# Performance work log

Measured on AMD Instinct MI355X. Metric: run time of the kernel, lower is better.

## Reference

```python
import jax, jax.numpy as jnp
import numpy as np
from jax import lax

B, BANDS, HW = 128, 30, 15
DIM, NH, NC = 512, 8, 16
EPS = 1e-5

def _ln(x, w, b):
    m = x.mean(-1, keepdims=True)
    v = ((x - m) ** 2).mean(-1, keepdims=True)
    return (x - m) / jnp.sqrt(v + EPS) * w + b

def _bn(x, g, b, m, v):
    # eval-mode BatchNorm2d over NCHW
    inv = g / jnp.sqrt(v + EPS)
    return x * inv[None, :, None, None] + (b - m * inv)[None, :, None, None]

def _conv(x, w, b):
    y = lax.conv_general_dilated(x, w, (1, 1), 'SAME', dimension_numbers=('NCHW', 'OIHW', 'NCHW'))
    return y + b[None, :, None, None]

def _attn(x, qkv_w, qkv_b, proj_w, proj_b):
    Bq, N, C = x.shape
    hd = C // NH
    qkv = (x @ qkv_w.T + qkv_b).reshape(Bq, N, 3, NH, hd).transpose(2, 0, 3, 1, 4)
    q, k, v = qkv[0], qkv[1], qkv[2]
    a = jax.nn.softmax(jnp.einsum('bhnd,bhmd->bhnm', q, k) * (hd ** -0.5), axis=-1)
    o = jnp.einsum('bhnm,bhmd->bhnd', a, v).transpose(0, 2, 1, 3).reshape(Bq, N, C)
    return o @ proj_w.T + proj_b

def _mlp(x, w1, b1, w2, b2):
    return jax.nn.gelu(x @ w1.T + b1, approximate=False) @ w2.T + b2

def _forward(x, conv_h_w, conv_h_b, bn_h_g, bn_h_b, bn_h_m, bn_h_v, cnn_conv_w, cnn_conv_b, cnn_bn_g, cnn_bn_b, cnn_bn_m, cnn_bn_v, cnn_fc_w, cnn_fc_b, spa_cls, spe_cls, spa_pos, spe_pos, blk_n1_w, blk_n1_b, blk_n2_w, blk_n2_b, blk_qkv_w, blk_qkv_b, blk_proj_w, blk_proj_b, blk_fc1_w, blk_fc1_b, blk_fc2_w, blk_fc2_b, norm1_w, norm1_b, norm2_w, norm2_b, head_w, head_b):
    x = x[:, 0]  # squeeze(1) -> [B, BANDS, H, W]
    Bn = x.shape[0]
    # --- spatial stream ---
    h = jax.nn.relu(_bn(_conv(x, conv_h_w, conv_h_b), bn_h_g, bn_h_b, bn_h_m, bn_h_v))
    spa = h.reshape(Bn, DIM, -1).transpose(0, 2, 1)  # b (h w) c
    spa = jnp.concatenate([jnp.broadcast_to(spa_cls, (Bn, 1, DIM)), spa], axis=1) + spa_pos
    # --- spectral stream: per-band CNN batched across bands in one pass ---
    bands = x.reshape(Bn * BANDS, 1, HW, HW)
    f = jax.nn.relu(_bn(_conv(bands, cnn_conv_w, cnn_conv_b), cnn_bn_g, cnn_bn_b, cnn_bn_m, cnn_bn_v))
    f = f.mean(axis=(2, 3))  # adaptive avg pool to 1x1
    f = jax.nn.relu(f @ cnn_fc_w.T + cnn_fc_b).reshape(Bn, BANDS, DIM)
    spe = jnp.concatenate([jnp.broadcast_to(spe_cls, (Bn, 1, DIM)), f], axis=1) + spe_pos
    xs, ys = spa, spe
    for i in range(2):  # CTMF blocks (eval: drop_path/dropout are identity)
        xin = _ln(jnp.concatenate([ys[:, :1], xs[:, 1:]], axis=1), blk_n1_w[i], blk_n1_b[i])
        yin = _ln(jnp.concatenate([xs[:, :1], ys[:, 1:]], axis=1), blk_n1_w[i], blk_n1_b[i])
        x_ = _attn(xin, blk_qkv_w[i], blk_qkv_b[i], blk_proj_w[i], blk_proj_b[i])
        y_ = _attn(yin, blk_qkv_w[i], blk_qkv_b[i], blk_proj_w[i], blk_proj_b[i])
        xs2 = xs + jnp.concatenate([xs[:, :1] + y_[:, :1], x_[:, 1:]], axis=1)
        ys2 = ys + jnp.concatenate([ys[:, :1] + x_[:, :1], y_[:, 1:]], axis=1)
        xs = xs2 + _mlp(_ln(xs2, blk_n2_w[i], blk_n2_b[i]), blk_fc1_w[i], blk_fc1_b[i], blk_fc2_w[i], blk_fc2_b[i])
        ys = ys2 + _mlp(_ln(ys2, blk_n2_w[i], blk_n2_b[i]), blk_fc1_w[i], blk_fc1_b[i], blk_fc2_w[i], blk_fc2_b[i])
    cls = jnp.concatenate([_ln(xs[:, 0], norm1_w, norm1_b), _ln(ys[:, 0], norm2_w, norm2_b)], axis=-1)
    return cls @ head_w.T + head_b

def setup_inputs() -> dict:
    key = jax.random.key(0)
    ks = jax.random.split(key, 32)
    r = lambda i, shape, s=0.02: jax.random.normal(ks[i], shape, dtype=jnp.float32) * s
    Nspa = HW * HW + 1
    Nspe = BANDS + 1
    return {
        'x': jax.random.normal(ks[0], (B, 1, BANDS, HW, HW), dtype=jnp.float32),
        'conv_h_w': r(1, (DIM, BANDS, 3, 3)),
        'conv_h_b': jnp.zeros((DIM,), jnp.float32),
        'bn_h_g': 1.0 + r(2, (DIM,)),
        'bn_h_b': r(3, (DIM,)),
        'bn_h_m': r(4, (DIM,), 0.1),
        'bn_h_v': 0.5 + jax.random.uniform(ks[5], (DIM,), dtype=jnp.float32),
        'cnn_conv_w': r(6, (128, 1, 3, 3), 0.1),
        'cnn_conv_b': jnp.zeros((128,), jnp.float32),
        'cnn_bn_g': 1.0 + r(7, (128,)),
        'cnn_bn_b': r(8, (128,)),
        'cnn_bn_m': r(9, (128,), 0.1),
        'cnn_bn_v': 0.5 + jax.random.uniform(ks[10], (128,), dtype=jnp.float32),
        'cnn_fc_w': r(11, (DIM, 128)),
        'cnn_fc_b': jnp.zeros((DIM,), jnp.float32),
        'spa_cls': jnp.zeros((1, 1, DIM), jnp.float32),
        'spe_cls': jnp.zeros((1, 1, DIM), jnp.float32),
        'spa_pos': r(12, (1, Nspa, DIM)),
        'spe_pos': r(13, (1, Nspe, DIM)),
        'blk_n1_w': jnp.ones((2, DIM), jnp.float32),
        'blk_n1_b': jnp.zeros((2, DIM), jnp.float32),
        'blk_n2_w': jnp.ones((2, DIM), jnp.float32),
        'blk_n2_b': jnp.zeros((2, DIM), jnp.float32),
        'blk_qkv_w': r(14, (2, 3 * DIM, DIM)),
        'blk_qkv_b': jnp.zeros((2, 3 * DIM), jnp.float32),
        'blk_proj_w': r(15, (2, DIM, DIM)),
        'blk_proj_b': jnp.zeros((2, DIM), jnp.float32),
        'blk_fc1_w': r(16, (2, DIM, DIM)),
        'blk_fc1_b': jnp.zeros((2, DIM), jnp.float32),
        'blk_fc2_w': r(17, (2, DIM, DIM)),
        'blk_fc2_b': jnp.zeros((2, DIM), jnp.float32),
        'norm1_w': jnp.ones((DIM,), jnp.float32),
        'norm1_b': jnp.zeros((DIM,), jnp.float32),
        'norm2_w': jnp.ones((DIM,), jnp.float32),
        'norm2_b': jnp.zeros((DIM,), jnp.float32),
        'head_w': r(18, (NC, 2 * DIM)),
        'head_b': jnp.zeros((NC,), jnp.float32),
    }

def reference(x, conv_h_w, conv_h_b, bn_h_g, bn_h_b, bn_h_m, bn_h_v, cnn_conv_w, cnn_conv_b, cnn_bn_g, cnn_bn_b, cnn_bn_m, cnn_bn_v, cnn_fc_w, cnn_fc_b, spa_cls, spe_cls, spa_pos, spe_pos, blk_n1_w, blk_n1_b, blk_n2_w, blk_n2_b, blk_qkv_w, blk_qkv_b, blk_proj_w, blk_proj_b, blk_fc1_w, blk_fc1_b, blk_fc2_w, blk_fc2_b, norm1_w, norm1_b, norm2_w, norm2_b, head_w, head_b):
    return _forward(x, conv_h_w, conv_h_b, bn_h_g, bn_h_b, bn_h_m, bn_h_v, cnn_conv_w, cnn_conv_b, cnn_bn_g, cnn_bn_b, cnn_bn_m, cnn_bn_v, cnn_fc_w, cnn_fc_b, spa_cls, spe_cls, spa_pos, spe_pos, blk_n1_w, blk_n1_b, blk_n2_w, blk_n2_b, blk_qkv_w, blk_qkv_b, blk_proj_w, blk_proj_b, blk_fc1_w, blk_fc1_b, blk_fc2_w, blk_fc2_b, norm1_w, norm1_b, norm2_w, norm2_b, head_w, head_b)
```

## Files before the change

### kernel.cpp

```cpp
#include <hip/hip_runtime.h>
#include <hip/hip_bf16.h>

typedef unsigned short u16;
typedef __attribute__((ext_vector_type(8))) short bf16x8;
typedef __attribute__((ext_vector_type(4))) float f32x4;

#define NB 128
#define BANDS 30
#define HWD 15
#define NPIX 225
#define DIMC 512
#define NHEAD 8
#define HD 64
#define NSPA 226
#define NSPE 31
#define EPSF 1e-5f
#define KCONV 320
#define MXROWS 28928
#define MYROWS 3968
#define M2ROWS 32896

__device__ __forceinline__ float b2f(u16 u) { return __uint_as_float(((unsigned)u) << 16); }
__device__ __forceinline__ u16 f2b(float f) {
  __hip_bfloat16 h = __float2bfloat16(f);
  return *reinterpret_cast<u16*>(&h);
}

#if __has_builtin(__builtin_amdgcn_global_load_lds)
#define HAVE_GLDS 1
__device__ __forceinline__ void gl_lds16(const void* g, void* l) {
  __builtin_amdgcn_global_load_lds((const __attribute__((address_space(1))) void*)g,
                                   (__attribute__((address_space(3))) void*)l, 16, 0, 0);
}
#else
#define HAVE_GLDS 0
#endif

__global__ __launch_bounds__(256) void cvt_k(const float* __restrict__ s, u16* __restrict__ d, int n) {
  for (int i = blockIdx.x * 256 + threadIdx.x; i < n; i += gridDim.x * 256) d[i] = f2b(s[i]);
}

__global__ __launch_bounds__(256) void convw_k(const float* __restrict__ w, u16* __restrict__ d) {
  int i = blockIdx.x * 256 + threadIdx.x;
  if (i >= DIMC * KCONV) return;
  int r = i / KCONV, c = i - r * KCONV;
  d[i] = (c < 270) ? f2b(w[r * 270 + c]) : (u16)0;
}

__global__ __launch_bounds__(256) void bnprep_k(const float* __restrict__ g, const float* __restrict__ bb,
    const float* __restrict__ bm, const float* __restrict__ bv, const float* __restrict__ cb,
    float* __restrict__ sc, float* __restrict__ sh) {
  int n = blockIdx.x * 256 + threadIdx.x;
  if (n < DIMC) {
    float inv = g[n] * rsqrtf(bv[n] + EPSF);
    sc[n] = inv;
    sh[n] = (cb[n] - bm[n]) * inv + bb[n];
  }
}

__global__ __launch_bounds__(256) void im2col_k(const float* __restrict__ x, u16* __restrict__ Ac) {
  int idx = blockIdx.x * 256 + threadIdx.x;
  if (idx >= 28800 * 40) return;
  int m = idx / 40, g = idx - m * 40;
  int b = m / NPIX, p = m - b * NPIX;
  int i = p / 15, j = p - i * 15;
  union { u16 v[8]; uint4 u; } out;
#pragma unroll
  for (int e = 0; e < 8; e++) {
    int c = g * 8 + e;
    float v = 0.f;
    if (c < 270) {
      int band = c / 9, q = c - band * 9;
      int di = q / 3, dj = q - di * 3;
      int ii = i + di - 1, jj = j + dj - 1;
      if ((unsigned)ii < 15u && (unsigned)jj < 15u)
        v = x[((size_t)b * BANDS + band) * NPIX + ii * 15 + jj];
    }
    out.v[e] = f2b(v);
  }
  *reinterpret_cast<uint4*>(Ac + (size_t)m * KCONV + g * 8) = out.u;
}

__global__ __launch_bounds__(256) void cls_init_k(const float* __restrict__ spa_cls,
    const float* __restrict__ spe_cls, const float* __restrict__ spa_pos,
    const float* __restrict__ spe_pos, float* __restrict__ xs, float* __restrict__ ys) {
  int b = blockIdx.x, t = threadIdx.x;
  int d0 = t, d1 = t + 256;
  xs[(size_t)b * NSPA * DIMC + d0] = spa_cls[d0] + spa_pos[d0];
  xs[(size_t)b * NSPA * DIMC + d1] = spa_cls[d1] + spa_pos[d1];
  ys[(size_t)b * NSPE * DIMC + d0] = spe_cls[d0] + spe_pos[d0];
  ys[(size_t)b * NSPE * DIMC + d1] = spe_cls[d1] + spe_pos[d1];
}

__global__ __launch_bounds__(256) void cnn_conv_k(const float* __restrict__ x,
    const float* __restrict__ w, const float* __restrict__ cb, const float* __restrict__ g,
    const float* __restrict__ bb, const float* __restrict__ bm, const float* __restrict__ bv,
    u16* __restrict__ pooled) {
  __shared__ float img[2][NPIX];
  int b0 = blockIdx.x * 2;
  int t = threadIdx.x;
  for (int idx = t; idx < 2 * NPIX; idx += 256) ((float*)img)[idx] = x[(size_t)b0 * NPIX + idx];
  __syncthreads();
  int half = t >> 7, ch = t & 127;
  const float* im = img[half];
  float inv = g[ch] * rsqrtf(bv[ch] + EPSF);
  float beta = bb[ch] - bm[ch] * inv;
  float w9[9];
#pragma unroll
  for (int q = 0; q < 9; q++) w9[q] = w[ch * 9 + q] * inv;
  float bias = cb[ch] * inv + beta;

  float rm[15], rc[15], rp[15];
#pragma unroll
  for (int j = 0; j < 15; j++) { rm[j] = 0.f; rc[j] = im[j]; }
  float sum = 0.f;
  for (int i = 0; i < 15; i++) {
#pragma unroll
    for (int j = 0; j < 15; j++) rp[j] = (i < 14) ? im[(i + 1) * 15 + j] : 0.f;
    float a[15];
#pragma unroll
    for (int j = 0; j < 15; j++) a[j] = fmaf(w9[4], rc[j], bias);
#pragma unroll
    for (int j = 0; j < 15; j++) {
      if (j > 0)  a[j] = fmaf(w9[3], rc[j - 1], a[j]);
      if (j < 14) a[j] = fmaf(w9[5], rc[j + 1], a[j]);
      a[j] = fmaf(w9[1], rm[j], a[j]);
      if (j > 0)  a[j] = fmaf(w9[0], rm[j - 1], a[j]);
      if (j < 14) a[j] = fmaf(w9[2], rm[j + 1], a[j]);
      a[j] = fmaf(w9[7], rp[j], a[j]);
      if (j > 0)  a[j] = fmaf(w9[6], rp[j - 1], a[j]);
      if (j < 14) a[j] = fmaf(w9[8], rp[j + 1], a[j]);
    }
#pragma unroll
    for (int j = 0; j < 15; j++) sum += fmaxf(a[j], 0.f);
#pragma unroll
    for (int j = 0; j < 15; j++) { rm[j] = rc[j]; rc[j] = rp[j]; }
  }
  pooled[(size_t)(b0 + half) * 128 + ch] = f2b(sum * (1.0f / 225.0f));
}

template <int GATHER>
__global__ __launch_bounds__(256) void ln_v_k(const float* __restrict__ xsc,
    const float* __restrict__ w, const float* __restrict__ bprm, u16* __restrict__ out) {
  int wid = threadIdx.x >> 6, lane = threadIdx.x & 63;
  int row = blockIdx.x * 4 + wid;
  const float* src;
  if (GATHER) {
    if (row < MXROWS) {
      int b = row / NSPA, tk = row - b * NSPA;
      src = (tk == 0) ? xsc + ((size_t)MXROWS + (size_t)b * NSPE) * DIMC
                      : xsc + (size_t)row * DIMC;
    } else {
      int ry = row - MXROWS;
      int b = ry / NSPE, tk = ry - b * NSPE;
      src = (tk == 0) ? xsc + (size_t)b * NSPA * DIMC : xsc + (size_t)row * DIMC;
    }
  } else {
    src = xsc + (size_t)row * DIMC;
  }
  float4 a0 = *reinterpret_cast<const float4*>(src + lane * 8);
  float4 a1 = *reinterpret_cast<const float4*>(src + lane * 8 + 4);
  float s = a0.x + a0.y + a0.z + a0.w + a1.x + a1.y + a1.z + a1.w;
  float sq = a0.x * a0.x + a0.y * a0.y + a0.z * a0.z + a0.w * a0.w +
             a1.x * a1.x + a1.y * a1.y + a1.z * a1.z + a1.w * a1.w;
#pragma unroll
  for (int off = 1; off <= 32; off <<= 1) { s += __shfl_xor(s, off); sq += __shfl_xor(sq, off); }
  float mean = s * (1.0f / 512.0f);
  float var = sq * (1.0f / 512.0f) - mean * mean;
  float rstd = rsqrtf(var + EPSF);
  float4 w0 = *reinterpret_cast<const float4*>(w + lane * 8);
  float4 w1 = *reinterpret_cast<const float4*>(w + lane * 8 + 4);
  float4 b0 = *reinterpret_cast<const float4*>(bprm + lane * 8);
  float4 b1 = *reinterpret_cast<const float4*>(bprm + lane * 8 + 4);
  union { u16 v[8]; uint4 u; } r;
  r.v[0] = f2b((a0.x - mean) * rstd * w0.x + b0.x);
  r.v[1] = f2b((a0.y - mean) * rstd * w0.y + b0.y);
  r.v[2] = f2b((a0.z - mean) * rstd * w0.z + b0.z);
  r.v[3] = f2b((a0.w - mean) * rstd * w0.w + b0.w);
  r.v[4] = f2b((a1.x - mean) * rstd * w1.x + b1.x);
  r.v[5] = f2b((a1.y - mean) * rstd * w1.y + b1.y);
  r.v[6] = f2b((a1.z - mean) * rstd * w1.z + b1.z);
  r.v[7] = f2b((a1.w - mean) * rstd * w1.w + b1.w);
  *reinterpret_cast<uint4*>(out + (size_t)row * DIMC + lane * 8) = r.u;
}

__global__ __launch_bounds__(256) void ln_cls_k(const float* __restrict__ xs,
    const float* __restrict__ ys, const float* __restrict__ w1, const float* __restrict__ b1,
    const float* __restrict__ w2, const float* __restrict__ b2, float* __restrict__ cls) {
  int gb = blockIdx.x;
  int half = gb & 1, b = gb >> 1;
  const float* src = half ? (ys + (size_t)b * NSPE * DIMC) : (xs + (size_t)b * NSPA * DIMC);
  const float* w = half ? w2 : w1;
  const float* bp = half ? b2 : b1;
  int t = threadIdx.x;
  float x0 = src[t], x1 = src[t + 256];
  float s = x0 + x1, sq = x0 * x0 + x1 * x1;
  for (int off = 32; off; off >>= 1) { s += __shfl_down(s, off); sq += __shfl_down(sq, off); }
  __shared__ float sa[4], sb4[4];
  int wid = t >> 6;
  if ((t & 63) == 0) { sa[wid] = s; sb4[wid] = sq; }
  __syncthreads();
  s = sa[0] + sa[1] + sa[2] + sa[3];
  sq = sb4[0] + sb4[1] + sb4[2] + sb4[3];
  float mean = s * (1.0f / 512.0f);
  float var = sq * (1.0f / 512.0f) - mean * mean;
  float rstd = rsqrtf(var + EPSF);
  cls[(size_t)b * 1024 + half * DIMC + t] = (x0 - mean) * rstd * w[t] + bp[t];
  cls[(size_t)b * 1024 + half * DIMC + t + 256] = (x1 - mean) * rstd * w[t + 256] + bp[t + 256];
}

template <int MODE>
__global__ __launch_bounds__(256) void mgemm_k(const u16* __restrict__ A, const u16* __restrict__ Bw,
    const float* __restrict__ bias, float* outf, u16* outb, int M, int N, int K,
    const float* aux0, const float* aux1, const float* aux2) {
  __shared__ u16 As[128 * 64];
  __shared__ u16 Bs[128 * 64];
  const int t = threadIdx.x;
  const int wid = t >> 6, l = t & 63;
  const int wm = wid >> 1, wn = wid & 1;
  const int fr = l & 15, kg = l >> 4;

  const int nx = gridDim.x, nwg = nx * gridDim.y;
  int hlin = blockIdx.y * nx + blockIdx.x;
  int xcd = hlin & 7, j = hlin >> 3;
  int q8 = nwg >> 3, r8 = nwg & 7;
  int L = (xcd < r8 ? xcd * (q8 + 1) : r8 * (q8 + 1) + (xcd - r8) * q8) + j;
  const int n0 = (L % nx) * 128, m0 = (L / nx) * 128;

  const int srow = l >> 3;
  const int sslot = l & 7;

  f32x4 acc[4][4];
#pragma unroll
  for (int i = 0; i < 4; i++)
#pragma unroll
    for (int j2 = 0; j2 < 4; j2++) acc[i][j2] = (f32x4){0.f, 0.f, 0.f, 0.f};

  for (int kq = 0; kq < K; kq += 64) {
#if !HAVE_GLDS
    uint4 ra[4], rb[4];
#pragma unroll
    for (int i = 0; i < 4; i++) {
      int r = wid * 32 + i * 8 + srow;
      int cg = sslot ^ (r & 7);
      ra[i] = *reinterpret_cast<const uint4*>(A + (size_t)(m0 + r) * K + kq + cg * 8);
      rb[i] = *reinterpret_cast<const uint4*>(Bw + (size_t)(n0 + r) * K + kq + cg * 8);
    }
#endif
    __syncthreads();
#if HAVE_GLDS
#pragma unroll
    for (int i = 0; i < 4; i++) {
      int r = wid * 32 + i * 8 + srow;
      int cg = sslot ^ (r & 7);
      gl_lds16(A + (size_t)(m0 + r) * K + kq + cg * 8, &As[(wid * 32 + i * 8) * 64]);
      gl_lds16(Bw + (size_t)(n0 + r) * K + kq + cg * 8, &Bs[(wid * 32 + i * 8) * 64]);
    }
#else
#pragma unroll
    for (int i = 0; i < 4; i++) {
      int r = wid * 32 + i * 8 + srow;
      *reinterpret_cast<uint4*>(&As[r * 64 + sslot * 8]) = ra[i];
      *reinterpret_cast<uint4*>(&Bs[r * 64 + sslot * 8]) = rb[i];
    }
#endif
    __syncthreads();
#pragma unroll
    for (int h = 0; h < 2; h++) {
      bf16x8 af[4], bfr[4];
#pragma unroll
      for (int mi = 0; mi < 4; mi++) {
        int r = wm * 64 + mi * 16 + fr;
        af[mi] = *reinterpret_cast<const bf16x8*>(&As[r * 64 + (((h * 4 + kg) ^ (fr & 7)) * 8)]);
      }
#pragma unroll
      for (int nj = 0; nj < 4; nj++) {
        int n = wn * 64 + nj * 16 + fr;
        bfr[nj] = *reinterpret_cast<const bf16x8*>(&Bs[n * 64 + (((h * 4 + kg) ^ (fr & 7)) * 8)]);
      }
#pragma unroll
      for (int mi = 0; mi < 4; mi++)
#pragma unroll
        for (int nj = 0; nj < 4; nj++)
          acc[mi][nj] = __builtin_amdgcn_mfma_f32_16x16x32_bf16(af[mi], bfr[nj], acc[mi][nj], 0, 0, 0);
    }
  }

#pragma unroll
  for (int mi = 0; mi < 4; mi++) {
#pragma unroll
    for (int q = 0; q < 4; q++) {
      int m = m0 + wm * 64 + mi * 16 + kg * 4 + q;
#pragma unroll
      for (int nj = 0; nj < 4; nj++) {
        int n = n0 + wn * 64 + nj * 16 + fr;
        float v = acc[mi][nj][q];
        if (MODE == 0) {
          outb[(size_t)m * N + n] = f2b(v + bias[n]);
        } else if (MODE == 1) {
          float z = v + bias[n];
          outb[(size_t)m * N + n] = f2b(0.5f * z * (1.0f + erff(z * 0.70710678118f)));
        } else if (MODE == 2) {
          size_t idx = (size_t)m * N + n;
          outf[idx] = v + bias[n] + aux0[idx];
        } else if (MODE == 3) {
          int b = m / NPIX, p = m - b * NPIX;
          float z = fmaxf(v * aux0[n] + aux1[n], 0.f) + aux2[(size_t)(p + 1) * DIMC + n];
          outf[((size_t)b * NSPA + p + 1) * DIMC + n] = z;
        } else if (MODE == 4) {
          int b = m / BANDS, band = m - b * BANDS;
          float z = fmaxf(v + bias[n], 0.f) + aux0[(size_t)(band + 1) * DIMC + n];
          outf[((size_t)b * NSPE + band + 1) * DIMC + n] = z;
        } else if (MODE == 5) {
          float z = v + bias[n];
          int tk, sidx;
          if (m < MXROWS) {
            int b = m / NSPA; tk = m - b * NSPA; sidx = b;
          } else {
            int ry = m - MXROWS; int b = ry / NSPE; tk = ry - b * NSPE; sidx = 128 + b;
          }
          if (tk == 0) outb[(size_t)sidx * DIMC + n] = f2b(z);
          else outf[(size_t)m * N + n] += z;
        }
      }
    }
  }
}

__global__ __launch_bounds__(256) void cls_swap_k(float* __restrict__ xsc,
                                                  const u16* __restrict__ clsprj) {
  int b = blockIdx.x, t = threadIdx.x;
  size_t xrow = (size_t)b * NSPA * DIMC;
  size_t yrow = ((size_t)MXROWS + (size_t)b * NSPE) * DIMC;
#pragma unroll
  for (int q = 0; q < 2; q++) {
    int d = t + q * 256;
    xsc[xrow + d] = 2.0f * xsc[xrow + d] + b2f(clsprj[(size_t)(128 + b) * DIMC + d]);
    xsc[yrow + d] = 2.0f * xsc[yrow + d] + b2f(clsprj[(size_t)b * DIMC + d]);
  }
}

template <int NTOK, int KP>
__global__ __launch_bounds__(256) void vt_k(const u16* __restrict__ qkv, u16* __restrict__ vtout) {
  __shared__ u16 Vl[64 * 72];
  int h = blockIdx.x, b = blockIdx.y;
  int t = threadIdx.x;
  const size_t rs = 3 * DIMC;
  const u16* src = qkv + (size_t)b * NTOK * rs + 2 * DIMC + h * HD;
  u16* dst = vtout + (size_t)(b * NHEAD + h) * HD * KP;
  for (int kt = 0; kt < KP / 64; kt++) {
    __syncthreads();
#pragma unroll
    for (int p = 0; p < 2; p++) {
      int idx = p * 256 + t;
      int row = idx >> 3, c = idx & 7;
      int tok = kt * 64 + row;
      uint4 v = make_uint4(0, 0, 0, 0);
      if (tok < NTOK) v = *reinterpret_cast<const uint4*>(src + (size_t)tok * rs + c * 8);
      *reinterpret_cast<uint4*>(&Vl[row * 72 + c * 8]) = v;
    }
    __syncthreads();
    int d = t & 63, tg = t >> 6;
    unsigned pu[8];
#pragma unroll
    for (int i = 0; i < 8; i++) {
      unsigned a = Vl[(tg * 16 + 2 * i) * 72 + d];
      unsigned bb2 = Vl[(tg * 16 + 2 * i + 1) * 72 + d];
      pu[i] = (bb2 << 16) | a;
    }
    uint4 o0 = make_uint4(pu[0], pu[1], pu[2], pu[3]);
    uint4 o1 = make_uint4(pu[4], pu[5], pu[6], pu[7]);
    u16* dp = dst + (size_t)d * KP + kt * 64 + tg * 16;
    *reinterpret_cast<uint4*>(dp) = o0;
    *reinterpret_cast<uint4*>(dp + 8) = o1;
  }
}

__device__ __forceinline__ int fsw(int row, int chunk) {
  return row * 64 + ((chunk ^ (row & 7)) << 3);
}
__device__ __forceinline__ void stage64(const u16* __restrict__ gsrc, size_t gstride,
                                        u16* lds, int w, int l) {
#pragma unroll
  for (int i = 0; i < 2; i++) {
    int r = w * 16 + i * 8 + (l >> 3);
    int c = l & 7;
    int scg = c ^ (r & 7);
    const u16* g = gsrc + (size_t)r * gstride + scg * 8;
#if HAVE_GLDS
    gl_lds16(g, &lds[(w * 16 + i * 8) * 64]);
#else
    *reinterpret_cast<uint4*>(&lds[r * 64 + c * 8]) = *reinterpret_cast<const uint4*>(g);
#endif
  }
}

__global__ __launch_bounds__(256) void flashq_k(const u16* __restrict__ qkv,
    const u16* __restrict__ vt, u16* __restrict__ o, int N, int kpad, float scale) {
  __shared__ u16 Qs[4][64 * 64];
  __shared__ u16 KV[2][64 * 64];
  u16* Ks = KV[0];
  u16* Vs = KV[1];
  u16* Ol = KV[0];
  const int h = blockIdx.x, b = blockIdx.y;
  const int t = threadIdx.x;
  const int w = t >> 6, l = t & 63;
  const int lr = l & 15, lk = l >> 4;
  const size_t rs = 3 * DIMC;
  const size_t qbase = (size_t)b * N * rs + h * HD;
  const u16* vbase = vt + (size_t)(b * NHEAD + h) * HD * kpad;

#pragma unroll
  for (int i = 0; i < 8; i++) {
    int r = i * 8 + (l >> 3);
    int c = l & 7;
    int scg = c ^ (r & 7);
    const u16* g = qkv + qbase + (size_t)(w * 64 + r) * rs + scg * 8;
#if HAVE_GLDS
    gl_lds16(g, &Qs[w][(i * 8) * 64]);
#else
    *reinterpret_cast<uint4*>(&Qs[w][r * 64 + c * 8]) = *reinterpret_cast<const uint4*>(g);
#endif
  }
  __syncthreads();
  bf16x8 bq[4][2];
#pragma unroll
  for (int nj = 0; nj < 4; nj++) {
    bq[nj][0] = *reinterpret_cast<const bf16x8*>(&Qs[w][fsw(nj * 16 + lr, lk)]);
    bq[nj][1] = *reinterpret_cast<const bf16x8*>(&Qs[w][fsw(nj * 16 + lr, 4 + lk)]);
  }

  float m_i[4], l_i[4];
  f32x4 oacc[4][4];
#pragma unroll
  for (int nj = 0; nj < 4; nj++) { m_i[nj] = -1e30f; l_i[nj] = 0.f; }
#pragma unroll
  for (int mi = 0; mi < 4; mi++)
#pragma unroll
    for (int nj = 0; nj < 4; nj++) oacc[mi][nj] = (f32x4){0.f, 0.f, 0.f, 0.f};

  const int nkt = kpad >> 6;
  for (int kt = 0; kt < nkt; kt++) {
    __syncthreads();
    stage64(qkv + qbase + DIMC + (size_t)(kt * 64) * rs, rs, Ks, w, l);
    stage64(vbase + kt * 64, (size_t)kpad, Vs, w, l);
    __syncthreads();

#pragma unroll
    for (int nj = 0; nj < 4; nj++) {
      f32x4 st[4];
#pragma unroll
      for (int mi = 0; mi < 4; mi++) st[mi] = (f32x4){0.f, 0.f, 0.f, 0.f};
      __builtin_amdgcn_s_setprio(1);
#pragma unroll
      for (int mi = 0; mi < 4; mi++) {
        bf16x8 ak0 = *reinterpret_cast<const bf16x8*>(&Ks[fsw(mi * 16 + lr, lk)]);
        bf16x8 ak1 = *reinterpret_cast<const bf16x8*>(&Ks[fsw(mi * 16 + lr, 4 + lk)]);
        st[mi] = __builtin_amdgcn_mfma_f32_16x16x32_bf16(ak0, bq[nj][0], st[mi], 0, 0, 0);
        st[mi] = __builtin_amdgcn_mfma_f32_16x16x32_bf16(ak1, bq[nj][1], st[mi], 0, 0, 0);
      }
      __builtin_amdgcn_s_setprio(0);

      float sv[4][4];
      float tmax = -1e30f;
#pragma unroll
      for (int mi = 0; mi < 4; mi++)
#pragma unroll
        for (int q = 0; q < 4; q++) {
          int kgl = kt * 64 + mi * 16 + lk * 4 + q;
          float v = (kgl < N) ? st[mi][q] * scale : -1e30f;
          sv[mi][q] = v;
          tmax = fmaxf(tmax, v);
        }
      tmax = fmaxf(tmax, __shfl_xor(tmax, 16));
      tmax = fmaxf(tmax, __shfl_xor(tmax, 32));
      float mn = fmaxf(m_i[nj], tmax);
      float corr = __expf(m_i[nj] - mn);
      m_i[nj] = mn;
      float rsum = 0.f;
#pragma unroll
      for (int mi = 0; mi < 4; mi++)
#pragma unroll
        for (int q = 0; q < 4; q++) {
          float p = __expf(sv[mi][q] - mn);
          sv[mi][q] = p;
          rsum += p;
        }
      rsum += __shfl_xor(rsum, 16);
      rsum += __shfl_xor(rsum, 32);
      l_i[nj] = l_i[nj] * corr + rsum;
#pragma unroll
      for (int mi = 0; mi < 4; mi++) oacc[mi][nj] *= corr;

      unsigned pk[4][2];
#pragma unroll
      for (int mi = 0; mi < 4; mi++) {
        pk[mi][0] = ((unsigned)f2b(sv[mi][1]) << 16) | (unsigned)f2b(sv[mi][0]);
        pk[mi][1] = ((unsigned)f2b(sv[mi][3]) << 16) | (unsigned)f2b(sv[mi][2]);
      }
      int src0 = lr + 32 * (lk & 1);
      int src1 = src0 + 16;
      bool hi = lk >= 2;
      bf16x8 pbv[2];
#pragma unroll
      for (int c = 0; c < 2; c++) {
        unsigned a0 = __shfl(pk[2 * c][0], src0), b0 = __shfl(pk[2 * c + 1][0], src0);
        unsigned a1 = __shfl(pk[2 * c][1], src0), b1 = __shfl(pk[2 * c + 1][1], src0);
        unsigned a2 = __shfl(pk[2 * c][0], src1), b2 = __shfl(pk[2 * c + 1][0], src1);
        unsigned a3 = __shfl(pk[2 * c][1], src1), b3 = __shfl(pk[2 * c + 1][1], src1);
        union { unsigned u[4]; bf16x8 v; } pu;
        pu.u[0] = hi ? b0 : a0;
        pu.u[1] = hi ? b1 : a1;
        pu.u[2] = hi ? b2 : a2;
        pu.u[3] = hi ? b3 : a3;
        pbv[c] = pu.v;
      }

      __builtin_amdgcn_s_setprio(1);
#pragma unroll
      for (int mi = 0; mi < 4; mi++) {
        bf16x8 av0 = *reinterpret_cast<const bf16x8*>(&Vs[fsw(mi * 16 + lr, lk)]);
        bf16x8 av1 = *reinterpret_cast<const bf16x8*>(&Vs[fsw(mi * 16 + lr, 4 + lk)]);
        oacc[mi][nj] = __builtin_amdgcn_mfma_f32_16x16x32_bf16(av0, pbv[0], oacc[mi][nj], 0, 0, 0);
        oacc[mi][nj] = __builtin_amdgcn_mfma_f32_16x16x32_bf16(av1, pbv[1], oacc[mi][nj], 0, 0, 0);
      }
      __builtin_amdgcn_s_setprio(0);
    }
  }

  float invl[4];
#pragma unroll
  for (int nj = 0; nj < 4; nj++) invl[nj] = 1.0f / l_i[nj];
  for (int pass = 0; pass < 4; pass++) {
    __syncthreads();
    if (w == pass) {
#pragma unroll
      for (int mi = 0; mi < 4; mi++)
#pragma unroll
        for (int nj = 0; nj < 4; nj++) {
          unsigned lo = ((unsigned)f2b(oacc[mi][nj][1] * invl[nj]) << 16) |
                        (unsigned)f2b(oacc[mi][nj][0] * invl[nj]);
          unsigned hi2 = ((unsigned)f2b(oacc[mi][nj][3] * invl[nj]) << 16) |
                         (unsigned)f2b(oacc[mi][nj][2] * invl[nj]);
          uint2 pr; pr.x = lo; pr.y = hi2;
          *reinterpret_cast<uint2*>(&Ol[(nj * 16 + lr) * 72 + mi * 16 + lk * 4]) = pr;
        }
    }
    __syncthreads();
    int row = t >> 2, c4 = t & 3;
    int qrow = pass * 64 + row;
    if (qrow < N) {
      uint4 v0 = *reinterpret_cast<const uint4*>(&Ol[row * 72 + c4 * 8]);
      uint4 v1 = *reinterpret_cast<const uint4*>(&Ol[row * 72 + (c4 + 4) * 8]);
      u16* op = o + ((size_t)b * N + qrow) * DIMC + h * HD;
      *reinterpret_cast<uint4*>(op + c4 * 8) = v0;
      *reinterpret_cast<uint4*>(op + (c4 + 4) * 8) = v1;
    }
  }
}

__global__ __launch_bounds__(256) void flashm_k(const u16* __restrict__ qkv,
    const u16* __restrict__ vt, u16* __restrict__ o, int N, int kpad, float scale) {
  __shared__ u16 Qs[64 * 64], Ks[64 * 64], Vs[64 * 64];
  __shared__ u16 Ol[64 * 72];
  const int qt = blockIdx.x, h = blockIdx.y, b = blockIdx.z;
  const int t = threadIdx.x;
  const int w = t >> 6, l = t & 63;
  const int lr = l & 15, lk = l >> 4;
  const size_t rs = 3 * DIMC;
  const size_t qbase = (size_t)b * N * rs + h * HD;
  const u16* vbase = vt + (size_t)(b * NHEAD + h) * HD * kpad;

  stage64(qkv + qbase + (size_t)(qt * 64) * rs, rs, Qs, w, l);
  __syncthreads();
  bf16x8 bq0 = *reinterpret_cast<const bf16x8*>(&Qs[fsw(w * 16 + lr, lk)]);
  bf16x8 bq1 = *reinterpret_cast<const bf16x8*>(&Qs[fsw(w * 16 + lr, 4 + lk)]);

  float m_i = -1e30f, l_i = 0.f;
  f32x4 oacc[4];
#pragma unroll
  for (int mi = 0; mi < 4; mi++) oacc[mi] = (f32x4){0.f, 0.f, 0.f, 0.f};

  const int nkt = (kpad + 63) >> 6;
  for (int kt = 0; kt < nkt; kt++) {
    __syncthreads();
    stage64(qkv + qbase + DIMC + (size_t)(kt * 64) * rs, rs, Ks, w, l);
    stage64(vbase + kt * 64, (size_t)kpad, Vs, w, l);
    __syncthreads();

    f32x4 st[4];
#pragma unroll
    for (int mi = 0; mi < 4; mi++) st[mi] = (f32x4){0.f, 0.f, 0.f, 0.f};
#pragma unroll
    for (int mi = 0; mi < 4; mi++) {
      bf16x8 ak0 = *reinterpret_cast<const bf16x8*>(&Ks[fsw(mi * 16 + lr, lk)]);
      bf16x8 ak1 = *reinterpret_cast<const bf16x8*>(&Ks[fsw(mi * 16 + lr, 4 + lk)]);
      st[mi] = __builtin_amdgcn_mfma_f32_16x16x32_bf16(ak0, bq0, st[mi], 0, 0, 0);
      st[mi] = __builtin_amdgcn_mfma_f32_16x16x32_bf16(ak1, bq1, st[mi], 0, 0, 0);
    }

    float sv[4][4];
    float tmax = -1e30f;
#pragma unroll
    for (int mi = 0; mi < 4; mi++)
#pragma unroll
      for (int q = 0; q < 4; q++) {
        int kgl = kt * 64 + mi * 16 + lk * 4 + q;
        float v = (kgl < N) ? st[mi][q] * scale : -1e30f;
        sv[mi][q] = v;
        tmax = fmaxf(tmax, v);
      }
    tmax = fmaxf(tmax, __shfl_xor(tmax, 16));
    tmax = fmaxf(tmax, __shfl_xor(tmax, 32));
    float mn = fmaxf(m_i, tmax);
    float corr = __expf(m_i - mn);
    m_i = mn;
    float rsum = 0.f;
#pragma unroll
    for (int mi = 0; mi < 4; mi++)
#pragma unroll
      for (int q = 0; q < 4; q++) {
        float p = __expf(sv[mi][q] - mn);
        sv[mi][q] = p;
        rsum += p;
      }
    rsum += __shfl_xor(rsum, 16);
    rsum += __shfl_xor(rsum, 32);
    l_i = l_i * corr + rsum;
#pragma unroll
    for (int mi = 0; mi < 4; mi++) oacc[mi] *= corr;

    unsigned pk[4][2];
#pragma unroll
    for (int mi = 0; mi < 4; mi++) {
      pk[mi][0] = ((unsigned)f2b(sv[mi][1]) << 16) | (unsigned)f2b(sv[mi][0]);
      pk[mi][1] = ((unsigned)f2b(sv[mi][3]) << 16) | (unsigned)f2b(sv[mi][2]);
    }
    int src0 = lr + 32 * (lk & 1);
    int src1 = src0 + 16;
    bool hi = lk >= 2;
    bf16x8 pbv[2];
#pragma unroll
    for (int c = 0; c < 2; c++) {
      unsigned a0 = __shfl(pk[2 * c][0], src0), b0 = __shfl(pk[2 * c + 1][0], src0);
      unsigned a1 = __shfl(pk[2 * c][1], src0), b1 = __shfl(pk[2 * c + 1][1], src0);
      unsigned a2 = __shfl(pk[2 * c][0], src1), b2 = __shfl(pk[2 * c + 1][0], src1);
      unsigned a3 = __shfl(pk[2 * c][1], src1), b3 = __shfl(pk[2 * c + 1][1], src1);
      union { unsigned u[4]; bf16x8 v; } pu;
      pu.u[0] = hi ? b0 : a0;
      pu.u[1] = hi ? b1 : a1;
      pu.u[2] = hi ? b2 : a2;
      pu.u[3] = hi ? b3 : a3;
      pbv[c] = pu.v;
    }

#pragma unroll
    for (int mi = 0; mi < 4; mi++) {
      bf16x8 av0 = *reinterpret_cast<const bf16x8*>(&Vs[fsw(mi * 16 + lr, lk)]);
      bf16x8 av1 = *reinterpret_cast<const bf16x8*>(&Vs[fsw(mi * 16 + lr, 4 + lk)]);
      oacc[mi] = __builtin_amdgcn_mfma_f32_16x16x32_bf16(av0, pbv[0], oacc[mi], 0, 0, 0);
      oacc[mi] = __builtin_amdgcn_mfma_f32_16x16x32_bf16(av1, pbv[1], oacc[mi], 0, 0, 0);
    }
  }

  float invl = 1.0f / l_i;
#pragma unroll
  for (int mi = 0; mi < 4; mi++) {
    unsigned lo = ((unsigned)f2b(oacc[mi][1] * invl) << 16) | (unsigned)f2b(oacc[mi][0] * invl);
    unsigned hi2 = ((unsigned)f2b(oacc[mi][3] * invl) << 16) | (unsigned)f2b(oacc[mi][2] * invl);
    uint2 pr; pr.x = lo; pr.y = hi2;
    *reinterpret_cast<uint2*>(&Ol[(w * 16 + lr) * 72 + mi * 16 + lk * 4]) = pr;
  }
  __syncthreads();
  {
    int row = t >> 2, c4 = t & 3;
    int qrow = qt * 64 + row;
    if (qrow < N) {
      uint4 v0 = *reinterpret_cast<const uint4*>(&Ol[row * 72 + c4 * 8]);
      uint4 v1 = *reinterpret_cast<const uint4*>(&Ol[row * 72 + (c4 + 4) * 8]);
      u16* op = o + ((size_t)b * N + qrow) * DIMC + h * HD;
      *reinterpret_cast<uint4*>(op + c4 * 8) = v0;
      *reinterpret_cast<uint4*>(op + (c4 + 4) * 8) = v1;
    }
  }
}

__global__ __launch_bounds__(256) void head_k(const float* __restrict__ cls,
    const float* __restrict__ hw, const float* __restrict__ hb, float* __restrict__ out) {
  __shared__ float cl[1024];
  __shared__ float part[256];
  int b = blockIdx.x, t = threadIdx.x;
  for (int idx = t; idx < 1024; idx += 256) cl[idx] = cls[(size_t)b * 1024 + idx];
  __syncthreads();
  int c = t >> 4, sl = t & 15;
  float p = 0.f;
  for (int j = 0; j < 64; j++) p += cl[sl * 64 + j] * hw[(size_t)c * 1024 + sl * 64 + j];
  part[t] = p;
  __syncthreads();
  if (sl == 0) {
    float sum = hb[c];
    for (int q = 0; q < 16; q++) sum += part[c * 16 + q];
    out[(size_t)b * 16 + c] = sum;
  }
}

extern "C" void kernel_launch(void* const* d_in, const int* in_sizes, int n_in,
                              void* d_out, int out_size, void* d_ws, size_t ws_size,
                              hipStream_t stream) {
  const float* x        = (const float*)d_in[0];
  const float* conv_h_w = (const float*)d_in[1];
  const float* conv_h_b = (const float*)d_in[2];
  const float* bn_h_g   = (const float*)d_in[3];
  const float* bn_h_b   = (const float*)d_in[4];
  const float* bn_h_m   = (const float*)d_in[5];
  const float* bn_h_v   = (const float*)d_in[6];
  const float* cnn_conv_w = (const float*)d_in[7];
  const float* cnn_conv_b = (const float*)d_in[8];
  const float* cnn_bn_g = (const float*)d_in[9];
  const float* cnn_bn_b = (const float*)d_in[10];
  const float* cnn_bn_m = (const float*)d_in[11];
  const float* cnn_bn_v = (const float*)d_in[12];
  const float* cnn_fc_w = (const float*)d_in[13];
  const float* cnn_fc_b = (const float*)d_in[14];
  const float* spa_cls  = (const float*)d_in[15];
  const float* spe_cls  = (const float*)d_in[16];
  const float* spa_pos  = (const float*)d_in[17];
  const float* spe_pos  = (const float*)d_in[18];
  const float* blk_n1_w = (const float*)d_in[19];
  const float* blk_n1_b = (const float*)d_in[20];
  const float* blk_n2_w = (const float*)d_in[21];
  const float* blk_n2_b = (const float*)d_in[22];
  const float* blk_qkv_w = (const float*)d_in[23];
  const float* blk_qkv_b = (const float*)d_in[24];
  const float* blk_proj_w = (const float*)d_in[25];
  const float* blk_proj_b = (const float*)d_in[26];
  const float* blk_fc1_w = (const float*)d_in[27];
  const float* blk_fc1_b = (const float*)d_in[28];
  const float* blk_fc2_w = (const float*)d_in[29];
  const float* blk_fc2_b = (const float*)d_in[30];
  const float* norm1_w  = (const float*)d_in[31];
  const float* norm1_b  = (const float*)d_in[32];
  const float* norm2_w  = (const float*)d_in[33];
  const float* norm2_b  = (const float*)d_in[34];
  const float* head_w   = (const float*)d_in[35];
  const float* head_b   = (const float*)d_in[36];

  char* ws = (char*)d_ws;
  size_t off = 0;
  auto take = [&](size_t bytes) -> char* {
    char* p = ws + off;
    off = (off + bytes + 255) & ~(size_t)255;
    return p;
  };
  const int Mx = MXROWS, M2 = M2ROWS;
  const int Mc = NB * NPIX;
  const int Mf = NB * BANDS;
  float* xsc  = (float*)take((size_t)M2 * DIMC * 4);
  float* ysb  = xsc + (size_t)Mx * DIMC;
  u16* xyin   = (u16*)take((size_t)M2 * DIMC * 2);
  u16* qkvxy  = (u16*)take((size_t)M2 * 3 * DIMC * 2);
  u16* oxy    = (u16*)take((size_t)M2 * DIMC * 2);
  u16* clsprj = (u16*)take((size_t)256 * DIMC * 2);
  float* clsb = (float*)take((size_t)NB * 1024 * 4);
  u16* pooled = (u16*)take((size_t)Mf * 128 * 2);
  u16* qkvWb  = (u16*)take((size_t)2 * 3 * DIMC * DIMC * 2);
  u16* projWb = (u16*)take((size_t)2 * DIMC * DIMC * 2);
  u16* fc1Wb  = (u16*)take((size_t)2 * DIMC * DIMC * 2);
  u16* fc2Wb  = (u16*)take((size_t)2 * DIMC * DIMC * 2);
  u16* fcWb   = (u16*)take((size_t)DIMC * 128 * 2);
  u16* convWb = (u16*)take((size_t)DIMC * KCONV * 2);
  float* bnsc = (float*)take(DIMC * 4);
  float* bnsh = (float*)take(DIMC * 4);
  u16* vty    = (u16*)take((size_t)NB * NHEAD * HD * 64 * 2);
  u16* Acol   = qkvxy;
  u16* vtx    = xyin;

  cvt_k<<<1024, 256, 0, stream>>>(blk_qkv_w, qkvWb, 2 * 3 * DIMC * DIMC);
  cvt_k<<<1024, 256, 0, stream>>>(blk_proj_w, projWb, 2 * DIMC * DIMC);
  cvt_k<<<1024, 256, 0, stream>>>(blk_fc1_w, fc1Wb, 2 * DIMC * DIMC);
  cvt_k<<<1024, 256, 0, stream>>>(blk_fc2_w, fc2Wb, 2 * DIMC * DIMC);
  cvt_k<<<256, 256, 0, stream>>>(cnn_fc_w, fcWb, DIMC * 128);
  convw_k<<<(DIMC * KCONV + 255) / 256, 256, 0, stream>>>(conv_h_w, convWb);
  bnprep_k<<<2, 256, 0, stream>>>(bn_h_g, bn_h_b, bn_h_m, bn_h_v, conv_h_b, bnsc, bnsh);

  cls_init_k<<<NB, 256, 0, stream>>>(spa_cls, spe_cls, spa_pos, spe_pos, xsc, ysb);
  im2col_k<<<(Mc * 40 + 255) / 256, 256, 0, stream>>>(x, Acol);
  mgemm_k<3><<<dim3(4, Mc / 128), 256, 0, stream>>>(Acol, convWb, nullptr, xsc, nullptr,
      Mc, DIMC, KCONV, bnsc, bnsh, spa_pos);
  cnn_conv_k<<<Mf / 2, 256, 0, stream>>>(x, cnn_conv_w, cnn_conv_b, cnn_bn_g, cnn_bn_b,
                                         cnn_bn_m, cnn_bn_v, pooled);
  mgemm_k<4><<<dim3(4, Mf / 128), 256, 0, stream>>>(pooled, fcWb, cnn_fc_b, ysb, nullptr,
      Mf, DIMC, 128, spe_pos, nullptr, nullptr);

  for (int i = 0; i < 2; i++) {
    const float* n1w = blk_n1_w + i * DIMC;
    const float* n1b = blk_n1_b + i * DIMC;
    const float* n2w = blk_n2_w + i * DIMC;
    const float* n2b = blk_n2_b + i * DIMC;
    const u16* qkvW = qkvWb + (size_t)i * 3 * DIMC * DIMC;
    const float* qkvB = blk_qkv_b + (size_t)i * 3 * DIMC;
    const u16* projW = projWb + (size_t)i * DIMC * DIMC;
    const float* projB = blk_proj_b + (size_t)i * DIMC;
    const u16* fc1W = fc1Wb + (size_t)i * DIMC * DIMC;
    const float* fc1B = blk_fc1_b + (size_t)i * DIMC;
    const u16* fc2W = fc2Wb + (size_t)i * DIMC * DIMC;
    const float* fc2B = blk_fc2_b + (size_t)i * DIMC;

    ln_v_k<1><<<M2 / 4, 256, 0, stream>>>(xsc, n1w, n1b, xyin);

    mgemm_k<0><<<dim3(12, M2 / 128), 256, 0, stream>>>(xyin, qkvW, qkvB, nullptr, qkvxy,
        M2, 3 * DIMC, DIMC, nullptr, nullptr, nullptr);

    vt_k<NSPA, 256><<<dim3(NHEAD, NB), 256, 0, stream>>>(qkvxy, vtx);
    vt_k<NSPE, 64><<<dim3(NHEAD, NB), 256, 0, stream>>>(qkvxy + (size_t)Mx * 3 * DIMC, vty);

    flashq_k<<<dim3(NHEAD, NB), 256, 0, stream>>>(qkvxy, vtx, oxy, NSPA, 256, 0.125f);
    flashm_k<<<dim3(1, NHEAD, NB), 256, 0, stream>>>(qkvxy + (size_t)Mx * 3 * DIMC, vty,
                                                     oxy + (size_t)Mx * DIMC, NSPE, 64, 0.125f);

    mgemm_k<5><<<dim3(4, M2 / 128), 256, 0, stream>>>(oxy, projW, projB, xsc, clsprj,
        M2, DIMC, DIMC, nullptr, nullptr, nullptr);
    cls_swap_k<<<NB, 256, 0, stream>>>(xsc, clsprj);

    ln_v_k<0><<<M2 / 4, 256, 0, stream>>>(xsc, n2w, n2b, xyin);
    mgemm_k<1><<<dim3(4, M2 / 128), 256, 0, stream>>>(xyin, fc1W, fc1B, nullptr, qkvxy,
        M2, DIMC, DIMC, nullptr, nullptr, nullptr);
    mgemm_k<2><<<dim3(4, M2 / 128), 256, 0, stream>>>(qkvxy, fc2W, fc2B, xsc, nullptr,
        M2, DIMC, DIMC, xsc, nullptr, nullptr);
  }

  ln_cls_k<<<NB * 2, 256, 0, stream>>>(xsc, ysb, norm1_w, norm1_b, norm2_w, norm2_b, clsb);
  head_k<<<NB, 256, 0, stream>>>(clsb, head_w, head_b, (float*)d_out);
}
```

Measured before the change: 830.7 us.

## Add 256x256-tile double-buffered GEMM kernel for transformer block matmuls

Adds a new g256_k GEMM with 256x256 output tiles, 512 threads and an XCD-aware block remapping. It uses double-buffered LDS staging through global_load_lds with an XOR-swizzled layout and raised wave priority around the MFMA loop. The QKV, projection, fc1 and fc2 GEMMs now use it instead of the 128-tile mgemm_k, and their epilogue modes move into the new kernel. The aim is more data reuse per tile and less global traffic. In exchange, activation buffers are padded to a multiple of 256 rows, and the large LDS footprint limits each CU to one block, with a partial wave on the N=512 GEMMs.

New measurement: 1.204 ms. 44.9% more time.

```diff
diff --git a/kernel.cpp b/kernel.cpp
--- a/kernel.cpp
+++ b/kernel.cpp
@@ -19,6 +19,7 @@
 #define MXROWS 28928
 #define MYROWS 3968
 #define M2ROWS 32896
+#define M2PAD 33024
 
 __device__ __forceinline__ float b2f(u16 u) { return __uint_as_float(((unsigned)u) << 16); }
 __device__ __forceinline__ u16 f2b(float f) {
@@ -295,15 +296,7 @@
       for (int nj = 0; nj < 4; nj++) {
         int n = n0 + wn * 64 + nj * 16 + fr;
         float v = acc[mi][nj][q];
-        if (MODE == 0) {
-          outb[(size_t)m * N + n] = f2b(v + bias[n]);
-        } else if (MODE == 1) {
-          float z = v + bias[n];
-          outb[(size_t)m * N + n] = f2b(0.5f * z * (1.0f + erff(z * 0.70710678118f)));
-        } else if (MODE == 2) {
-          size_t idx = (size_t)m * N + n;
-          outf[idx] = v + bias[n] + aux0[idx];
-        } else if (MODE == 3) {
+        if (MODE == 3) {
           int b = m / NPIX, p = m - b * NPIX;
           float z = fmaxf(v * aux0[n] + aux1[n], 0.f) + aux2[(size_t)(p + 1) * DIMC + n];
           outf[((size_t)b * NSPA + p + 1) * DIMC + n] = z;
@@ -311,16 +304,132 @@
           int b = m / BANDS, band = m - b * BANDS;
           float z = fmaxf(v + bias[n], 0.f) + aux0[(size_t)(band + 1) * DIMC + n];
           outf[((size_t)b * NSPE + band + 1) * DIMC + n] = z;
-        } else if (MODE == 5) {
-          float z = v + bias[n];
-          int tk, sidx;
-          if (m < MXROWS) {
-            int b = m / NSPA; tk = m - b * NSPA; sidx = b;
-          } else {
-            int ry = m - MXROWS; int b = ry / NSPE; tk = ry - b * NSPE; sidx = 128 + b;
+        }
+      }
+    }
+  }
+}
+
+template <int MODE>
+__global__ __launch_bounds__(512, 2) void g256_k(const u16* __restrict__ A,
+    const u16* __restrict__ Bw, const float* __restrict__ bias, float* outf, u16* outb,
+    int M, int N, int K, const float* aux0) {
+  __shared__ u16 As[2][256 * 64];
+  __shared__ u16 Bs[2][256 * 64];
+  const int t = threadIdx.x;
+  const int w = t >> 6, l = t & 63;
+  const int wm = w >> 2, wn = w & 3;
+  const int fr = l & 15, kg = l >> 4;
+
+  const int nx = gridDim.x, nwg = nx * gridDim.y;
+  int hlin = blockIdx.y * nx + blockIdx.x;
+  int xcd = hlin & 7, jj = hlin >> 3;
+  int q8 = nwg >> 3, r8 = nwg & 7;
+  int L = (xcd < r8 ? xcd * (q8 + 1) : r8 * (q8 + 1) + (xcd - r8) * q8) + jj;
+  const int n0 = (L % nx) * 256, m0 = (L / nx) * 256;
+
+  const int srow = l >> 3;
+  const int sslot = l & 7;
+  const int scg = sslot ^ srow;
+
+  f32x4 acc[8][4];
+#pragma unroll
+  for (int i = 0; i < 8; i++)
+#pragma unroll
+    for (int j2 = 0; j2 < 4; j2++) acc[i][j2] = (f32x4){0.f, 0.f, 0.f, 0.f};
+
+  const int nkt = K >> 6;
+
+  auto STAGE = [&](int buf, int kt) {
+    const int kq = kt * 64;
+#pragma unroll
+    for (int i = 0; i < 4; i++) {
+      int rb = w * 32 + i * 8;
+#if HAVE_GLDS
+      gl_lds16(A + (size_t)(m0 + rb + srow) * K + kq + scg * 8, &As[buf][rb * 64]);
+      gl_lds16(Bw + (size_t)(n0 + rb + srow) * K + kq + scg * 8, &Bs[buf][rb * 64]);
+#else
+      *reinterpret_cast<uint4*>(&As[buf][(rb + srow) * 64 + scg * 8]) =
+          *reinterpret_cast<const uint4*>(A + (size_t)(m0 + rb + srow) * K + kq + sslot * 8);
+      *reinterpret_cast<uint4*>(&Bs[buf][(rb + srow) * 64 + scg * 8]) =
+          *reinterpret_cast<const uint4*>(Bw + (size_t)(n0 + rb + srow) * K + kq + sslot * 8);
+#endif
+    }
+  };
+
+  STAGE(0, 0);
+  STAGE(1, 1);
+  asm volatile("s_waitcnt vmcnt(8)" ::: "memory");
+  __builtin_amdgcn_s_barrier();
+
+  for (int kt = 0; kt < nkt; kt++) {
+    const int buf = kt & 1;
+    const u16* Ab = As[buf];
+    const u16* Bb = Bs[buf];
+#pragma unroll
+    for (int kh = 0; kh < 2; kh++) {
+      bf16x8 af[8], bfr[4];
+#pragma unroll
+      for (int mi = 0; mi < 8; mi++) {
+        int r = wm * 128 + mi * 16 + fr;
+        af[mi] = *reinterpret_cast<const bf16x8*>(&Ab[r * 64 + (((kh * 4 + kg) ^ (fr & 7)) << 3)]);
+      }
+#pragma unroll
+      for (int nj = 0; nj < 4; nj++) {
+        int n = wn * 64 + nj * 16 + fr;
+        bfr[nj] = *reinterpret_cast<const bf16x8*>(&Bb[n * 64 + (((kh * 4 + kg) ^ (fr & 7)) << 3)]);
+      }
+      __builtin_amdgcn_s_setprio(1);
+#pragma unroll
+      for (int mi = 0; mi < 8; mi++)
+#pragma unroll
+        for (int nj = 0; nj < 4; nj++)
+          acc[mi][nj] = __builtin_amdgcn_mfma_f32_16x16x32_bf16(af[mi], bfr[nj], acc[mi][nj], 0, 0, 0);
+      __builtin_amdgcn_s_setprio(0);
+    }
+    asm volatile("s_waitcnt lgkmcnt(0)" ::: "memory");
+    __builtin_amdgcn_sched_barrier(0);
+    __builtin_amdgcn_s_barrier();
+    if (kt + 2 < nkt) STAGE(buf, kt + 2);
+    if (kt + 1 < nkt) {
+      if (kt + 2 < nkt) {
+        asm volatile("s_waitcnt vmcnt(8)" ::: "memory");
+      } else {
+        asm volatile("s_waitcnt vmcnt(0)" ::: "memory");
+      }
+      __builtin_amdgcn_s_barrier();
+    }
+  }
+
+#pragma unroll
+  for (int mi = 0; mi < 8; mi++) {
+#pragma unroll
+    for (int q = 0; q < 4; q++) {
+      int m = m0 + wm * 128 + mi * 16 + kg * 4 + q;
+      if (m < M) {
+#pragma unroll
+        for (int nj = 0; nj < 4; nj++) {
+          int n = n0 + wn * 64 + nj * 16 + fr;
+          float v = acc[mi][nj][q];
+          if (MODE == 0) {
+            outb[(size_t)m * N + n] = f2b(v + bias[n]);
+          } else if (MODE == 1) {
+            float z = v + bias[n];
+            outb[(size_t)m * N + n] = f2b(0.5f * z * (1.0f + erff(z * 0.70710678118f)));
+          } else if (MODE == 2) {
+            size_t idx = (size_t)m * N + n;
+            outf[idx] = v + bias[n] + aux0[idx];
+          } else if (MODE == 5) {
+            float z = v + bias[n];
+            int tk, sidx;
+            if (m < MXROWS) {
+              int b = m / NSPA; tk = m - b * NSPA; sidx = b;
+            } else {
+              int ry = m - MXROWS; int b = ry / NSPE; tk = ry - b * NSPE; sidx = 128 + b;
+            }
+            if (tk == 0) outb[(size_t)sidx * DIMC + n] = f2b(z);
+            else outf[(size_t)m * N + n] += z;
           }
-          if (tk == 0) outb[(size_t)sidx * DIMC + n] = f2b(z);
-          else outf[(size_t)m * N + n] += z;
         }
       }
     }
@@ -757,9 +866,9 @@
   const int Mf = NB * BANDS;
   float* xsc  = (float*)take((size_t)M2 * DIMC * 4);
   float* ysb  = xsc + (size_t)Mx * DIMC;
-  u16* xyin   = (u16*)take((size_t)M2 * DIMC * 2);
-  u16* qkvxy  = (u16*)take((size_t)M2 * 3 * DIMC * 2);
-  u16* oxy    = (u16*)take((size_t)M2 * DIMC * 2);
+  u16* xyin   = (u16*)take((size_t)M2PAD * DIMC * 2);
+  u16* qkvxy  = (u16*)take((size_t)M2PAD * 3 * DIMC * 2);
+  u16* oxy    = (u16*)take((size_t)M2PAD * DIMC * 2);
   u16* clsprj = (u16*)take((size_t)256 * DIMC * 2);
   float* clsb = (float*)take((size_t)NB * 1024 * 4);
   u16* pooled = (u16*)take((size_t)Mf * 128 * 2);
@@ -808,8 +917,8 @@
 
     ln_v_k<1><<<M2 / 4, 256, 0, stream>>>(xsc, n1w, n1b, xyin);
 
-    mgemm_k<0><<<dim3(12, M2 / 128), 256, 0, stream>>>(xyin, qkvW, qkvB, nullptr, qkvxy,
-        M2, 3 * DIMC, DIMC, nullptr, nullptr, nullptr);
+    g256_k<0><<<dim3(6, M2PAD / 256), 512, 0, stream>>>(xyin, qkvW, qkvB, nullptr, qkvxy,
+        M2, 3 * DIMC, DIMC, nullptr);
 
     vt_k<NSPA, 256><<<dim3(NHEAD, NB), 256, 0, stream>>>(qkvxy, vtx);
     vt_k<NSPE, 64><<<dim3(NHEAD, NB), 256, 0, stream>>>(qkvxy + (size_t)Mx * 3 * DIMC, vty);
@@ -818,15 +927,15 @@
     flashm_k<<<dim3(1, NHEAD, NB), 256, 0, stream>>>(qkvxy + (size_t)Mx * 3 * DIMC, vty,
                                                      oxy + (size_t)Mx * DIMC, NSPE, 64, 0.125f);
 
-    mgemm_k<5><<<dim3(4, M2 / 128), 256, 0, stream>>>(oxy, projW, projB, xsc, clsprj,
-        M2, DIMC, DIMC, nullptr, nullptr, nullptr);
+    g256_k<5><<<dim3(2, M2PAD / 256), 512, 0, stream>>>(oxy, projW, projB, xsc, clsprj,
+        M2, DIMC, DIMC, nullptr);
     cls_swap_k<<<NB, 256, 0, stream>>>(xsc, clsprj);
 
     ln_v_k<0><<<M2 / 4, 256, 0, stream>>>(xsc, n2w, n2b, xyin);
-    mgemm_k<1><<<dim3(4, M2 / 128), 256, 0, stream>>>(xyin, fc1W, fc1B, nullptr, qkvxy,
-        M2, DIMC, DIMC, nullptr, nullptr, nullptr);
-    mgemm_k<2><<<dim3(4, M2 / 128), 256, 0, stream>>>(qkvxy, fc2W, fc2B, xsc, nullptr,
-        M2, DIMC, DIMC, xsc, nullptr, nullptr);
+    g256_k<1><<<dim3(2, M2PAD / 256), 512, 0, stream>>>(xyin, fc1W, fc1B, nullptr, qkvxy,
+        M2, DIMC, DIMC, nullptr);
+    g256_k<2><<<dim3(2, M2PAD / 256), 512, 0, stream>>>(qkvxy, fc2W, fc2B, xsc, nullptr,
+        M2, DIMC, DIMC, xsc);
   }
 
   ln_cls_k<<<NB * 2, 256, 0, stream>>>(xsc, ysb, norm1_w, norm1_b, norm2_w, norm2_b, clsb);
```
